# Kernel tuning notes

Hardware: AMD Instinct MI355X
Metric: run time of the kernel (lower is better)

Reference implementation:

```python
import jax, jax.numpy as jnp
import numpy as np

LN_EPS = 1e-5


def conv2d(x, w, b, stride, pad):
    # x: NCHW, w: OIHW
    y = jax.lax.conv_general_dilated(
        x, w, (stride, stride), [(pad, pad), (pad, pad)],
        dimension_numbers=("NCHW", "OIHW", "NCHW"))
    return y + b[None, :, None, None]


def gdn(x, gamma, beta):
    # y_c = x_c / sqrt(beta_c + sum_j gamma_cj * x_j^2)  (1x1 conv on x^2)
    norm = jnp.einsum("bchw,dc->bdhw", x * x, gamma) + beta[None, :, None, None]
    return x / jnp.sqrt(norm)


def layernorm(x, w, b):
    mu = jnp.mean(x, axis=-1, keepdims=True)
    var = jnp.var(x, axis=-1, keepdims=True)
    return (x - mu) / jnp.sqrt(var + LN_EPS) * w + b


def setup_inputs() -> dict:
    key = jax.random.key(0)
    ks = jax.random.split(key, 16)
    r = lambda i, shape: (jax.random.normal(ks[i], shape) * 0.02).astype(jnp.float32)
    N, M, K, D = 128, 192, 192, 128
    return {
        "x_p": jax.random.normal(ks[0], (4, 16, 3, 64, 64), jnp.float32),
        "y_g": jax.random.normal(ks[1], (64, K, 32), jnp.float32),
        "conv1_w": r(2, (N, 3, 5, 5)), "conv1_b": jnp.zeros((N,), jnp.float32),
        "gamma1": (0.1 * jnp.eye(N) + 1e-3).astype(jnp.float32), "beta1": jnp.ones((N,), jnp.float32),
        "conv2_w": r(3, (N, N, 5, 5)), "conv2_b": jnp.zeros((N,), jnp.float32),
        "gamma2": (0.1 * jnp.eye(N) + 1e-3).astype(jnp.float32), "beta2": jnp.ones((N,), jnp.float32),
        "conv3_w": r(4, (M, N, 3, 3)), "conv3_b": jnp.zeros((M,), jnp.float32),
        "ln_q_w": jnp.ones((M,), jnp.float32), "ln_q_b": jnp.zeros((M,), jnp.float32),
        "ln_kv_w": jnp.ones((K,), jnp.float32), "ln_kv_b": jnp.zeros((K,), jnp.float32),
        "ln_out_w": jnp.ones((M,), jnp.float32), "ln_out_b": jnp.zeros((M,), jnp.float32),
        "Wq": r(5, (D, M)), "Wk": r(6, (D, K)), "v_w": r(7, (1, D)),
        "Wv": r(8, (M, K)), "out_w": r(9, (M, M)), "out_b": jnp.zeros((M,), jnp.float32),
    }


def reference(x_p, y_g, conv1_w, conv1_b, gamma1, beta1, conv2_w, conv2_b,
              gamma2, beta2, conv3_w, conv3_b, ln_q_w, ln_q_b, ln_kv_w, ln_kv_b,
              ln_out_w, ln_out_b, Wq, Wk, v_w, Wv, out_w, out_b):
    B, P, C, Hp, Wp = x_p.shape
    x = x_p.reshape(B * P, C, Hp, Wp)
    # local encoder: conv s2 -> GDN -> conv s2 -> GDN -> conv s1 k3
    x = gdn(conv2d(x, conv1_w, conv1_b, 2, 2), gamma1, beta1)
    x = gdn(conv2d(x, conv2_w, conv2_b, 2, 2), gamma2, beta2)
    y_local = conv2d(x, conv3_w, conv3_b, 1, 1)          # (BP, M, h, w)
    BP, M, h, w = y_local.shape
    q = y_local.reshape(BP, M, h * w).transpose(0, 2, 1)  # (BP, Tq, M)
    kv = y_g.reshape(BP, y_g.shape[1], -1).transpose(0, 2, 1)  # (BP, Tk, K)
    q = layernorm(q, ln_q_w, ln_q_b)
    kv = layernorm(kv, ln_kv_w, ln_kv_b)
    # Bahdanau additive attention
    q_proj = jnp.einsum("bqm,dm->bqd", q, Wq)            # (BP, Tq, D)
    k_proj = jnp.einsum("bkc,dc->bkd", kv, Wk)           # (BP, Tk, D)
    energy = jnp.einsum("bqkd,d->bqk",
                        jnp.tanh(q_proj[:, :, None, :] + k_proj[:, None, :, :]),
                        v_w[0])                           # (BP, Tq, Tk)
    alpha = jax.nn.softmax(energy, axis=-1)
    v_proj = jnp.einsum("bkc,mc->bkm", kv, Wv)           # (BP, Tk, M)
    context = jnp.einsum("bqk,bkm->bqm", alpha, v_proj)
    context = jnp.einsum("bqm,nm->bqn", context, out_w) + out_b
    fused = layernorm(q + context, ln_out_w, ln_out_b)
    return fused.transpose(0, 2, 1).reshape(BP, M, h, w)
```

## Files before the change

kernel.cpp:

```cpp
#include <hip/hip_runtime.h>
#include <cstddef>
#include <cstdint>


typedef __bf16 bf16x8 __attribute__((ext_vector_type(8)));
typedef float floatx4 __attribute__((ext_vector_type(4)));
typedef unsigned short ushortT;
typedef unsigned short ushort8v __attribute__((ext_vector_type(8)));

#if __has_builtin(__builtin_amdgcn_exp2f)
#define EXP2F(x) __builtin_amdgcn_exp2f(x)
#else
#define EXP2F(x) exp2f(x)
#endif
#if __has_builtin(__builtin_amdgcn_rcpf)
#define RCPF(x) __builtin_amdgcn_rcpf(x)
#else
#define RCPF(x) (1.f / (x))
#endif

__device__ __forceinline__ ushortT f2bf(float f) {
  unsigned u = __builtin_bit_cast(unsigned, f);
  unsigned r = (u + 0x7FFFu + ((u >> 16) & 1u)) >> 16;
  return (ushortT)r;
}
__device__ __forceinline__ float bf2f(ushortT u) {
  return __builtin_bit_cast(float, ((unsigned)u) << 16);
}

static constexpr size_t OFF_T1BF = 0;
static constexpr size_t OFF_X2BF = 4194304;
static constexpr size_t OFF_T2BF = 8388608;
static constexpr size_t OFF_X3BF = 9437184;
static constexpr size_t OFF_QRAW = 10485760;
static constexpr size_t OFF_WBQ  = 21299200;
static constexpr size_t OFF_WBK  = 21311488;
static constexpr size_t OFF_WBV  = 21323776;
static constexpr size_t OFF_WBO  = 21342208;
static constexpr size_t OFF_WT2  = 26079232;
static constexpr size_t OFF_WT3  = 26284032;
static constexpr size_t OFF_WC1  = 26394624;
static constexpr size_t OFF_GB1  = 26406912;
static constexpr size_t OFF_GB2  = 26415104;

__device__ __constant__ int d_TWI2[4][9] = {{ 0, 2, 4,10,12,14,20,22,24},
                                            { 1, 3,11,13,21,23, 0, 0, 0},
                                            { 5, 7, 9,15,17,19, 0, 0, 0},
                                            { 6, 8,16,18, 0, 0, 0, 0, 0}};
__device__ __constant__ int d_NT2[4] = {9, 6, 6, 4};

__device__ void dev_convw3(const float* w, ushortT* wt, int mode, int total,
                           int idx) {
  if (idx >= total) return;
  int j    = idx & 7;
  int om   = (idx >> 3) & 63;
  int kg   = (idx >> 9) & 3;
  int slab = idx >> 11;
  int mt, s, tap, T;
  if (mode == 0) {
    int ph;
    if (slab < 72) ph = 0; else if (slab < 120) ph = 1;
    else if (slab < 168) ph = 2; else ph = 3;
    const int st[4] = {0, 72, 120, 168};
    const int ns[4] = {36, 24, 24, 16};
    int rel = slab - st[ph];
    mt = rel / ns[ph]; s = rel % ns[ph];
    tap = d_TWI2[ph][s >> 2]; T = 25;
  } else {
    mt = slab / 36; s = slab % 36; tap = s >> 2; T = 9;
  }
  int cc = s & 3;
  int c  = cc * 32 + kg * 8 + j;
  int oc = mt * 64 + om;
  wt[idx] = f2bf(w[(size_t)(oc * 128 + c) * T + tap]);
}

__device__ void dev_convw1(const float* w, ushortT* wt, int idx) {
  if (idx >= 20480) return;
  int k    = idx & 31;
  int oc   = (idx >> 5) & 127;
  int slab = idx >> 12;
  int ph, i;
  if (slab < 2) { ph = 0; i = slab; } else { ph = slab - 1; i = 0; }
  int kg = k >> 3, jj = k & 7;
  int tidx = i * 8 + jj;
  float val = 0.f;
  if (kg < 3 && tidx < d_NT2[ph]) {
    int tap = d_TWI2[ph][tidx];
    val = w[(size_t)(oc * 3 + kg) * 25 + tap];
  }
  wt[idx] = f2bf(val);
}

__device__ void dev_wcast(const float* w, ushortT* wb, int total, float scale,
                          int idx) {
  if (idx < total) wb[idx] = f2bf(w[idx] * scale);
}

__global__ __launch_bounds__(256) void prep_kernel(
    const float* __restrict__ conv2_w, ushortT* __restrict__ wt2,
    const float* __restrict__ conv3_w, ushortT* __restrict__ wt3,
    const float* __restrict__ conv1_w, ushortT* __restrict__ wc1,
    const float* __restrict__ Wq, ushortT* __restrict__ wbq,
    const float* __restrict__ Wk, ushortT* __restrict__ wbk,
    const float* __restrict__ Wv, ushortT* __restrict__ wbv,
    const float* __restrict__ out_w, ushortT* __restrict__ wbo,
    const float* __restrict__ gamma1, ushortT* __restrict__ gb1,
    const float* __restrict__ gamma2, ushortT* __restrict__ gb2) {
  constexpr float C2LE = 2.88539008177792681f;
  int blk = blockIdx.x, tid = threadIdx.x;
  if (blk < 1600)      dev_convw3(conv2_w, wt2, 0, 409600, blk * 256 + tid);
  else if (blk < 2464) dev_convw3(conv3_w, wt3, 1, 221184, (blk - 1600) * 256 + tid);
  else if (blk < 2544) dev_convw1(conv1_w, wc1, (blk - 2464) * 256 + tid);
  else if (blk < 2640) dev_wcast(Wq, wbq, 24576, C2LE, (blk - 2544) * 256 + tid);
  else if (blk < 2736) dev_wcast(Wk, wbk, 24576, C2LE, (blk - 2640) * 256 + tid);
  else if (blk < 2880) dev_wcast(Wv, wbv, 36864, 1.f, (blk - 2736) * 256 + tid);
  else if (blk < 3024) dev_wcast(out_w, wbo, 36864, 1.f, (blk - 2880) * 256 + tid);
  else if (blk < 3088) dev_wcast(gamma1, gb1, 16384, 1.f, (blk - 3024) * 256 + tid);
  else                 dev_wcast(gamma2, gb2, 16384, 1.f, (blk - 3088) * 256 + tid);
}

__global__ __launch_bounds__(256, 1) void conv1_mfma_kernel(
    const float* __restrict__ x, const ushortT* __restrict__ wc1,
    const float* __restrict__ bias, ushortT* __restrict__ outb) {
  int b  = blockIdx.x >> 2;
  int yg = blockIdx.x & 3;
  int y0 = yg * 8;

  int wave = threadIdx.x >> 6;
  int lane = threadIdx.x & 63;
  int ln15 = lane & 15;
  int kg   = lane >> 4;
  int tid  = threadIdx.x;

  __shared__ ushortT simg[4680];
  __shared__ ushortT sA[5 * 128 * 40];

  for (int j = tid; j < 2340; j += 256) ((unsigned*)simg)[j] = 0u;
  __syncthreads();

  int ihBase = 2 * y0 - 2;
  const float* xb = x + (size_t)b * 3 * 4096;
  for (int j = tid; j < 960; j += 256) {
    int q = j & 15;
    int rr = j >> 4;
    int c = rr / 20, ihl = rr % 20;
    int ih = ihBase + ihl;
    if (ih >= 0 && ih < 64) {
      float4 v = *(const float4*)&xb[c * 4096 + ih * 64 + q * 4];
      int pr = ih & 1, u = ih >> 1;
      int lr = u - y0 + 1;
      int base0 = ((pr * 2 + 0) * 3 + c) * 360 + lr * 36;
      int base1 = ((pr * 2 + 1) * 3 + c) * 360 + lr * 36;
      simg[base0 + 2 * q + 1] = f2bf(v.x);
      simg[base1 + 2 * q + 1] = f2bf(v.y);
      simg[base0 + 2 * q + 2] = f2bf(v.z);
      simg[base1 + 2 * q + 2] = f2bf(v.w);
    }
  }
  for (int j = tid; j < 2560; j += 256) {
    int chunk = j & 3, row = j >> 2;
    uint4 v = *(const uint4*)&wc1[row * 32 + chunk * 8];
    *(uint4*)&sA[row * 40 + chunk * 8] = v;
  }
  __syncthreads();

  constexpr int TDR[4][9] = {{-1,-1,-1, 0, 0, 0, 1, 1, 1},
                             {-1,-1, 0, 0, 1, 1, 0, 0, 0},
                             {-1,-1,-1, 0, 0, 0, 0, 0, 0},
                             {-1,-1, 0, 0, 0, 0, 0, 0, 0}};
  constexpr int TDC[4][9] = {{-1, 0, 1,-1, 0, 1,-1, 0, 1},
                             {-1, 0,-1, 0,-1, 0, 0, 0, 0},
                             {-1, 0, 1,-1, 0, 1, 0, 0, 0},
                             {-1, 0,-1, 0, 0, 0, 0, 0, 0}};
  constexpr int NT[4]  = {9, 6, 6, 4};
  constexpr int NM[4]  = {2, 1, 1, 1};
  constexpr int SB[4]  = {0, 2, 3, 4};

  ushort8v Bf[4][5];
  #pragma unroll
  for (int ntl = 0; ntl < 4; ++ntl) {
    int ntg = wave * 4 + ntl;
    int yloc = ntg >> 1;
    int xx = (ntg & 1) * 16 + ln15;
    int lbase = (yloc + 1) * 36 + xx + 1 + kg * 360;
    #pragma unroll
    for (int ph = 0; ph < 4; ++ph) {
      int pbase = ph * 1080 + lbase;
      #pragma unroll
      for (int i = 0; i < 2; ++i) {
        if (i < NM[ph]) {
          ushort8v bv;
          #pragma unroll
          for (int j = 0; j < 8; ++j) {
            int tidx = i * 8 + j;
            if (tidx >= NT[ph]) tidx = 0;
            int off = TDR[ph][tidx] * 36 + TDC[ph][tidx];
            bv[j] = simg[pbase + off];
          }
          Bf[ntl][SB[ph] + i] = bv;
        }
      }
    }
  }

  #pragma unroll
  for (int m = 0; m < 8; ++m) {
    bf16x8 Af[5];
    #pragma unroll
    for (int s = 0; s < 5; ++s)
      Af[s] = *(const bf16x8*)&sA[(s * 128 + m * 16 + ln15) * 40 + kg * 8];
    int oc0 = m * 16 + kg * 4;
    float4 bv = *(const float4*)&bias[oc0];
    #pragma unroll
    for (int ntl = 0; ntl < 4; ++ntl) {
      floatx4 acc = (floatx4)0.f;
      #pragma unroll
      for (int s = 0; s < 5; ++s)
        acc = __builtin_amdgcn_mfma_f32_16x16x32_bf16(
            Af[s], __builtin_bit_cast(bf16x8, Bf[ntl][s]), acc, 0, 0, 0);
      int ntg = wave * 4 + ntl;
      int y = y0 + (ntg >> 1);
      int xx = (ntg & 1) * 16 + ln15;
      int p = y * 32 + xx;
      ushort4 o4 = {f2bf(acc[0] + bv.x), f2bf(acc[1] + bv.y),
                    f2bf(acc[2] + bv.z), f2bf(acc[3] + bv.w)};
      *(ushort4*)&outb[((size_t)b * 1024 + p) * 128 + oc0] = o4;
    }
  }
}

__global__ __launch_bounds__(256) void gdn_mfma_kernel(
    const ushortT* __restrict__ xbf, const ushortT* __restrict__ gb,
    const float* __restrict__ beta, ushortT* __restrict__ ybf,
    int HW, int nPixTiles, int isSplit) {
  int pt = blockIdx.x % nPixTiles;
  int b  = blockIdx.x / nPixTiles;
  int px0 = pt * 64;
  int tid = threadIdx.x;
  int wave = tid >> 6, lane = tid & 63, ln15 = lane & 15, kg = lane >> 4;

  __shared__ ushortT sG[128 * 136];
  __shared__ ushortT sX[64 * 136];

  for (int j = tid; j < 2048; j += 256) {
    int row = j >> 4, ch = j & 15;
    *(uint4*)&sG[row * 136 + ch * 8] = *(const uint4*)&gb[row * 128 + ch * 8];
  }
  for (int j = tid; j < 1024; j += 256) {
    int row = j >> 4, ch = j & 15;
    ushort8v xv = *(const ushort8v*)&xbf[((size_t)(b * HW + px0 + row)) * 128 + ch * 8];
    ushort8v sq;
    #pragma unroll
    for (int r = 0; r < 8; ++r) {
      float f = bf2f(xv[r]);
      sq[r] = f2bf(f * f);
    }
    *(ushort8v*)&sX[row * 136 + ch * 8] = sq;
  }
  __syncthreads();

  floatx4 acc[2][4];
  #pragma unroll
  for (int mi = 0; mi < 2; ++mi)
    #pragma unroll
    for (int nt = 0; nt < 4; ++nt) acc[mi][nt] = (floatx4)0.f;

  #pragma unroll
  for (int k0 = 0; k0 < 128; k0 += 32) {
    bf16x8 a0 = *(const bf16x8*)&sG[(wave * 32 + ln15) * 136 + k0 + kg * 8];
    bf16x8 a1 = *(const bf16x8*)&sG[(wave * 32 + 16 + ln15) * 136 + k0 + kg * 8];
    #pragma unroll
    for (int nt = 0; nt < 4; ++nt) {
      bf16x8 bb = *(const bf16x8*)&sX[(nt * 16 + ln15) * 136 + k0 + kg * 8];
      acc[0][nt] = __builtin_amdgcn_mfma_f32_16x16x32_bf16(a0, bb, acc[0][nt], 0, 0, 0);
      acc[1][nt] = __builtin_amdgcn_mfma_f32_16x16x32_bf16(a1, bb, acc[1][nt], 0, 0, 0);
    }
  }

  #pragma unroll
  for (int mi = 0; mi < 2; ++mi) {
    int d0 = wave * 32 + mi * 16 + kg * 4;
    float4 bt = *(const float4*)&beta[d0];
    #pragma unroll
    for (int nt = 0; nt < 4; ++nt) {
      int p = px0 + nt * 16 + ln15;
      ushort4 x4 = *(const ushort4*)&xbf[((size_t)(b * HW + p)) * 128 + d0];
      ushort4 o4;
      o4.x = f2bf(bf2f(x4.x) * rsqrtf(acc[mi][nt][0] + bt.x));
      o4.y = f2bf(bf2f(x4.y) * rsqrtf(acc[mi][nt][1] + bt.y));
      o4.z = f2bf(bf2f(x4.z) * rsqrtf(acc[mi][nt][2] + bt.z));
      o4.w = f2bf(bf2f(x4.w) * rsqrtf(acc[mi][nt][3] + bt.w));
      size_t dst;
      if (isSplit) {
        int h = p >> 5, w5 = p & 31;
        int ph = ((h & 1) << 1) | (w5 & 1);
        dst = (((size_t)b * 4 + ph) * 256 + (h >> 1) * 16 + (w5 >> 1)) * 128 + d0;
      } else {
        dst = ((size_t)b * 256 + p) * 128 + d0;
      }
      *(ushort4*)&ybf[dst] = o4;
    }
  }
}

template<int MODE>
__global__ __launch_bounds__(256, 2) void conv_mfma_kernel(
    const ushortT* __restrict__ X,
    const ushortT* __restrict__ Wt,
    const float* __restrict__ bias,
    ushortT* __restrict__ outb) {
  constexpr int OC  = (MODE == 0) ? 128 : 192;
  constexpr int NMT = OC / 64;
  constexpr int NPH = (MODE == 0) ? 4 : 1;

  int b   = blockIdx.x / (NMT * 4);
  int rem = blockIdx.x % (NMT * 4);
  int mt  = rem >> 2;
  int rs  = rem & 3;
  int r0  = rs * 4;

  int wave = threadIdx.x >> 6;
  int lane = threadIdx.x & 63;
  int ln15 = lane & 15;
  int kg   = lane >> 4;

  __shared__ ushortT simg[6 * 18 * 136];

  floatx4 acc[4];
  #pragma unroll
  for (int m = 0; m < 4; ++m) acc[m] = (floatx4)0.f;

  constexpr int NS2[4]      = {36, 24, 24, 16};
  constexpr int PHSTART2[4] = {0, 72, 120, 168};
  constexpr int TDR_2[4][9] = {{-1,-1,-1, 0, 0, 0, 1, 1, 1},
                               {-1,-1, 0, 0, 1, 1, 0, 0, 0},
                               {-1,-1,-1, 0, 0, 0, 0, 0, 0},
                               {-1,-1, 0, 0, 0, 0, 0, 0, 0}};
  constexpr int TDC_2[4][9] = {{-1, 0, 1,-1, 0, 1,-1, 0, 1},
                               {-1, 0,-1, 0,-1, 0, 0, 0, 0},
                               {-1, 0, 1,-1, 0, 1, 0, 0, 0},
                               {-1, 0,-1, 0, 0, 0, 0, 0, 0}};
  constexpr int TDR_3[9] = {-1,-1,-1, 0, 0, 0, 1, 1, 1};
  constexpr int TDC_3[9] = {-1, 0, 1,-1, 0, 1,-1, 0, 1};

  const int aoff = kg * 512 + ln15 * 8;
  uint4 apf[8][4];

  #pragma unroll
  for (int ph = 0; ph < NPH; ++ph) {
    const int NS = (MODE == 0) ? NS2[ph] : 36;
    const int slabBase = (MODE == 0) ? (PHSTART2[ph] + mt * NS2[ph]) : (mt * 36);
    const ushortT* wp0 = Wt + (size_t)slabBase * 2048 + aoff;

    __syncthreads();
    const ushortT* Xb = X + (((size_t)b * NPH + ph) * 256) * 128;
    for (int idx = threadIdx.x; idx < 1728; idx += 256) {
      int chunk = idx & 15;
      int pix = idx >> 4;
      int row = pix / 18, colm = pix - row * 18;
      int i = r0 - 1 + row, j = colm - 1;
      uint4 v = {0u, 0u, 0u, 0u};
      if (i >= 0 && i < 16 && j >= 0 && j < 16)
        v = *(const uint4*)(Xb + ((size_t)(i * 16 + j)) * 128 + chunk * 8);
      *(uint4*)&simg[(row * 18 + colm) * 136 + chunk * 8] = v;
    }
    #pragma unroll
    for (int jj = 0; jj < 8; ++jj)
      if (jj < NS) {
        #pragma unroll
        for (int m = 0; m < 4; ++m)
          apf[jj][m] = *(const uint4*)(wp0 + (size_t)jj * 2048 + m * 128);
      }
    __syncthreads();

    #pragma unroll
    for (int s0 = 0; s0 < NS; s0 += 8) {
      #pragma unroll
      for (int jj = 0; jj < 8; ++jj) {
        int s = s0 + jj;
        if (s < NS) {
          bf16x8 acur[4];
          #pragma unroll
          for (int m = 0; m < 4; ++m) acur[m] = __builtin_bit_cast(bf16x8, apf[jj][m]);
          int sp = s + 8;
          if (sp < NS) {
            #pragma unroll
            for (int m = 0; m < 4; ++m)
              apf[jj][m] = *(const uint4*)(wp0 + (size_t)sp * 2048 + m * 128);
          }
          int t  = s >> 2;
          int c0 = (s & 3) * 32;
          int dr = (MODE == 0) ? TDR_2[ph][t] : TDR_3[t];
          int dc = (MODE == 0) ? TDC_2[ph][t] : TDC_3[t];
          int lrow = wave + dr + 1;
          int lcol = ln15 + dc + 1;
          bf16x8 bfr = *(const bf16x8*)&simg[(lrow * 18 + lcol) * 136 + c0 + kg * 8];
          #pragma unroll
          for (int m = 0; m < 4; ++m)
            acc[m] = __builtin_amdgcn_mfma_f32_16x16x32_bf16(acur[m], bfr, acc[m], 0, 0, 0);
        }
      }
    }
  }

  #pragma unroll
  for (int m = 0; m < 4; ++m) {
    int mg = mt * 64 + m * 16 + kg * 4;
    float4 bv = *(const float4*)&bias[mg];
    int r = r0 + wave;
    int p = r * 16 + ln15;
    ushort4 o4 = {f2bf(acc[m][0] + bv.x), f2bf(acc[m][1] + bv.y),
                  f2bf(acc[m][2] + bv.z), f2bf(acc[m][3] + bv.w)};
    *(ushort4*)&outb[((size_t)b * 256 + p) * OC + mg] = o4;
  }
}

__global__ __launch_bounds__(256) void attn_mega_kernel(
    const ushortT* __restrict__ qrawb, const float* __restrict__ ln_q_w,
    const float* __restrict__ ln_q_b, const float* __restrict__ yg,
    const float* __restrict__ ln_kv_w, const float* __restrict__ ln_kv_b,
    const ushortT* __restrict__ wbq, const ushortT* __restrict__ wbk,
    const ushortT* __restrict__ wbv, const ushortT* __restrict__ wbo,
    const float* __restrict__ vw, const float* __restrict__ out_b,
    const float* __restrict__ ln_out_w, const float* __restrict__ ln_out_b,
    float* __restrict__ out) {
  __shared__ ushortT smem[37640];
  ushortT* sqln   = smem;
  ushortT* skv    = smem + 6400;
  float*   skvRaw = (float*)(smem + 12800);
  float*   sqpF   = (float*)(smem + 12800);
  float*   skpF   = (float*)(smem + 21248);
  ushortT* svpT   = smem + 29696;
  float*   swm    = (float*)(smem + 37376);
  float*   sS0    = (float*)(smem + 37632);
  float*   se     = (float*)(smem + 6400);
  ushortT* sctx   = smem + 12800;
  float*   sf     = (float*)(smem + 21248);

  int b  = blockIdx.x >> 3;
  int t0 = (blockIdx.x & 7) * 32;
  int tid  = threadIdx.x;
  int wave = tid >> 6;
  int lane = tid & 63;
  int ln15 = lane & 15;
  int kg   = lane >> 4;

  {
    const float4* yg4 = (const float4*)(yg + (size_t)b * 6144);
    for (int j = tid; j < 1536; j += 256) {
      float4 v = yg4[j];
      int c = j >> 3;
      int t4 = (j & 7) * 4;
      skvRaw[(t4 + 0) * 194 + c] = v.x;
      skvRaw[(t4 + 1) * 194 + c] = v.y;
      skvRaw[(t4 + 2) * 194 + c] = v.z;
      skvRaw[(t4 + 3) * 194 + c] = v.w;
    }
  }
  for (int r = wave; r < 32; r += 4) {
    const ushortT* xr = qrawb + ((size_t)(b * 256 + t0 + r)) * 192;
    float v0 = bf2f(xr[lane]), v1 = bf2f(xr[lane + 64]), v2 = bf2f(xr[lane + 128]);
    float s = v0 + v1 + v2;
    float s2 = v0 * v0 + v1 * v1 + v2 * v2;
    #pragma unroll
    for (int off = 32; off; off >>= 1) { s += __shfl_xor(s, off); s2 += __shfl_xor(s2, off); }
    float mean = s * (1.f / 192.f);
    float var = s2 * (1.f / 192.f) - mean * mean;
    float inv = rsqrtf(var + 1e-5f);
    sqln[r * 200 + lane]       = f2bf((v0 - mean) * inv * ln_q_w[lane]       + ln_q_b[lane]);
    sqln[r * 200 + lane + 64]  = f2bf((v1 - mean) * inv * ln_q_w[lane + 64]  + ln_q_b[lane + 64]);
    sqln[r * 200 + lane + 128] = f2bf((v2 - mean) * inv * ln_q_w[lane + 128] + ln_q_b[lane + 128]);
  }
  if (tid < 128) swm[tid] = -2.f * vw[tid];
  if (tid >= 128 && tid < 192) {
    int l = tid - 128;
    float s = vw[l] + vw[l + 64];
    #pragma unroll
    for (int off = 32; off; off >>= 1) s += __shfl_xor(s, off);
    if (l == 0) *sS0 = s;
  }
  __syncthreads();

  for (int r = wave; r < 32; r += 4) {
    const float* src = skvRaw + r * 194;
    float v0 = src[lane], v1 = src[lane + 64], v2 = src[lane + 128];
    float s = v0 + v1 + v2;
    float s2 = v0 * v0 + v1 * v1 + v2 * v2;
    #pragma unroll
    for (int off = 32; off; off >>= 1) { s += __shfl_xor(s, off); s2 += __shfl_xor(s2, off); }
    float mean = s * (1.f / 192.f);
    float var = s2 * (1.f / 192.f) - mean * mean;
    float inv = rsqrtf(var + 1e-5f);
    skv[r * 200 + lane]       = f2bf((v0 - mean) * inv * ln_kv_w[lane]       + ln_kv_b[lane]);
    skv[r * 200 + lane + 64]  = f2bf((v1 - mean) * inv * ln_kv_w[lane + 64]  + ln_kv_b[lane + 64]);
    skv[r * 200 + lane + 128] = f2bf((v2 - mean) * inv * ln_kv_w[lane + 128] + ln_kv_b[lane + 128]);
  }
  __syncthreads();

  for (int ti = wave; ti < 56; ti += 4) {
    floatx4 acc = (floatx4)0.f;
    if (ti < 16) {
      int rt = ti >> 3, ct = ti & 7;
      #pragma unroll
      for (int k0 = 0; k0 < 192; k0 += 32) {
        bf16x8 afr = *(const bf16x8*)&sqln[(rt * 16 + ln15) * 200 + k0 + kg * 8];
        bf16x8 bfr = *(const bf16x8*)&wbq[((size_t)(ct * 16 + ln15)) * 192 + k0 + kg * 8];
        acc = __builtin_amdgcn_mfma_f32_16x16x32_bf16(afr, bfr, acc, 0, 0, 0);
      }
      #pragma unroll
      for (int r = 0; r < 4; ++r)
        sqpF[(rt * 16 + kg * 4 + r) * 132 + ct * 16 + ln15] = acc[r];
    } else if (ti < 32) {
      int t2 = ti - 16;
      int rt = t2 >> 3, ct = t2 & 7;
      #pragma unroll
      for (int k0 = 0; k0 < 192; k0 += 32) {
        bf16x8 afr = *(const bf16x8*)&skv[(rt * 16 + ln15) * 200 + k0 + kg * 8];
        bf16x8 bfr = *(const bf16x8*)&wbk[((size_t)(ct * 16 + ln15)) * 192 + k0 + kg * 8];
        acc = __builtin_amdgcn_mfma_f32_16x16x32_bf16(afr, bfr, acc, 0, 0, 0);
      }
      #pragma unroll
      for (int r = 0; r < 4; ++r)
        skpF[(rt * 16 + kg * 4 + r) * 132 + ct * 16 + ln15] = acc[r];
    } else {
      int t2 = ti - 32;
      int rt = t2 / 12, ct = t2 % 12;
      #pragma unroll
      for (int k0 = 0; k0 < 192; k0 += 32) {
        bf16x8 afr = *(const bf16x8*)&skv[(rt * 16 + ln15) * 200 + k0 + kg * 8];
        bf16x8 bfr = *(const bf16x8*)&wbv[((size_t)(ct * 16 + ln15)) * 192 + k0 + kg * 8];
        acc = __builtin_amdgcn_mfma_f32_16x16x32_bf16(afr, bfr, acc, 0, 0, 0);
      }
      #pragma unroll
      for (int r = 0; r < 4; ++r)
        svpT[(ct * 16 + ln15) * 40 + rt * 16 + kg * 4 + r] = f2bf(acc[r]);
    }
  }
  __syncthreads();

  {
    float S0v = *sS0;
    int qq0 = tid >> 4, kc = tid & 15;
    const float4* w4 = (const float4*)swm;
    #pragma unroll
    for (int st = 0; st < 2; ++st) {
      int qq = st * 16 + qq0;
      const float4* q4 = (const float4*)&sqpF[qq * 132];
      const float4* ka = (const float4*)&skpF[kc * 132];
      const float4* kb = (const float4*)&skpF[(kc + 16) * 132];
      float acc0 = S0v, acc1 = S0v;
      #pragma unroll 8
      for (int d4 = 0; d4 < 32; ++d4) {
        float4 qv = q4[d4], k0v = ka[d4], k1v = kb[d4], wv = w4[d4];
        acc0 += wv.x * RCPF(EXP2F(qv.x + k0v.x) + 1.f);
        acc0 += wv.y * RCPF(EXP2F(qv.y + k0v.y) + 1.f);
        acc0 += wv.z * RCPF(EXP2F(qv.z + k0v.z) + 1.f);
        acc0 += wv.w * RCPF(EXP2F(qv.w + k0v.w) + 1.f);
        acc1 += wv.x * RCPF(EXP2F(qv.x + k1v.x) + 1.f);
        acc1 += wv.y * RCPF(EXP2F(qv.y + k1v.y) + 1.f);
        acc1 += wv.z * RCPF(EXP2F(qv.z + k1v.z) + 1.f);
        acc1 += wv.w * RCPF(EXP2F(qv.w + k1v.w) + 1.f);
      }
      se[qq * 36 + kc] = acc0;
      se[qq * 36 + kc + 16] = acc1;
    }
  }
  __syncthreads();

  if (tid < 32) {
    float* ser = se + tid * 36;
    float mx = -1e30f;
    for (int k = 0; k < 32; ++k) mx = fmaxf(mx, ser[k]);
    float s = 0.f;
    for (int k = 0; k < 32; ++k) { float a = __expf(ser[k] - mx); ser[k] = a; s += a; }
    float invs = 1.f / s;
    for (int k = 0; k < 32; ++k) ser[k] *= invs;
  }
  __syncthreads();

  for (int ti = wave; ti < 24; ti += 4) {
    int rt = ti / 12, ct = ti % 12;
    float4 a0 = *(const float4*)&se[(rt * 16 + ln15) * 36 + kg * 8];
    float4 a1 = *(const float4*)&se[(rt * 16 + ln15) * 36 + kg * 8 + 4];
    ushort8v au;
    au[0] = f2bf(a0.x); au[1] = f2bf(a0.y); au[2] = f2bf(a0.z); au[3] = f2bf(a0.w);
    au[4] = f2bf(a1.x); au[5] = f2bf(a1.y); au[6] = f2bf(a1.z); au[7] = f2bf(a1.w);
    bf16x8 bfr = *(const bf16x8*)&svpT[(ct * 16 + ln15) * 40 + kg * 8];
    floatx4 acc = __builtin_amdgcn_mfma_f32_16x16x32_bf16(
        __builtin_bit_cast(bf16x8, au), bfr, (floatx4)0.f, 0, 0, 0);
    #pragma unroll
    for (int r = 0; r < 4; ++r)
      sctx[(rt * 16 + kg * 4 + r) * 200 + ct * 16 + ln15] = f2bf(acc[r]);
  }
  __syncthreads();

  for (int ti = wave; ti < 24; ti += 4) {
    int rt = ti / 12, ct = ti % 12;
    floatx4 acc = (floatx4)0.f;
    #pragma unroll
    for (int k0 = 0; k0 < 192; k0 += 32) {
      bf16x8 afr = *(const bf16x8*)&sctx[(rt * 16 + ln15) * 200 + k0 + kg * 8];
      bf16x8 bfr = *(const bf16x8*)&wbo[((size_t)(ct * 16 + ln15)) * 192 + k0 + kg * 8];
      acc = __builtin_amdgcn_mfma_f32_16x16x32_bf16(afr, bfr, acc, 0, 0, 0);
    }
    float bv = out_b[ct * 16 + ln15];
    #pragma unroll
    for (int r = 0; r < 4; ++r)
      sf[(rt * 16 + kg * 4 + r) * 193 + ct * 16 + ln15] = acc[r] + bv;
  }
  __syncthreads();

  for (int rr = wave; rr < 32; rr += 4) {
    int t = t0 + rr;
    const ushortT* xr = qrawb + ((size_t)(b * 256 + t)) * 192;
    float r0_ = bf2f(xr[lane]), r1_ = bf2f(xr[lane + 64]), r2_ = bf2f(xr[lane + 128]);
    float s = r0_ + r1_ + r2_;
    float s2 = r0_ * r0_ + r1_ * r1_ + r2_ * r2_;
    #pragma unroll
    for (int off = 32; off; off >>= 1) { s += __shfl_xor(s, off); s2 += __shfl_xor(s2, off); }
    float mean = s * (1.f / 192.f);
    float var = s2 * (1.f / 192.f) - mean * mean;
    float inv = rsqrtf(var + 1e-5f);
    float q0 = (r0_ - mean) * inv * ln_q_w[lane]       + ln_q_b[lane];
    float q1 = (r1_ - mean) * inv * ln_q_w[lane + 64]  + ln_q_b[lane + 64];
    float q2 = (r2_ - mean) * inv * ln_q_w[lane + 128] + ln_q_b[lane + 128];
    float v0 = sf[rr * 193 + lane]       + q0;
    float v1 = sf[rr * 193 + lane + 64]  + q1;
    float v2 = sf[rr * 193 + lane + 128] + q2;
    float t_s = v0 + v1 + v2;
    float t_s2 = v0 * v0 + v1 * v1 + v2 * v2;
    #pragma unroll
    for (int off = 32; off; off >>= 1) { t_s += __shfl_xor(t_s, off); t_s2 += __shfl_xor(t_s2, off); }
    float m2 = t_s * (1.f / 192.f);
    float var2 = t_s2 * (1.f / 192.f) - m2 * m2;
    float inv2 = rsqrtf(var2 + 1e-5f);
    sf[rr * 193 + lane]       = (v0 - m2) * inv2 * ln_out_w[lane]       + ln_out_b[lane];
    sf[rr * 193 + lane + 64]  = (v1 - m2) * inv2 * ln_out_w[lane + 64]  + ln_out_b[lane + 64];
    sf[rr * 193 + lane + 128] = (v2 - m2) * inv2 * ln_out_w[lane + 128] + ln_out_b[lane + 128];
  }
  __syncthreads();

  for (int j = tid; j < 1536; j += 256) {
    int m = j >> 3, t4 = j & 7;
    float4 o4;
    o4.x = sf[(t4 * 4 + 0) * 193 + m];
    o4.y = sf[(t4 * 4 + 1) * 193 + m];
    o4.z = sf[(t4 * 4 + 2) * 193 + m];
    o4.w = sf[(t4 * 4 + 3) * 193 + m];
    *(float4*)&out[((size_t)(b * 192 + m)) * 256 + t0 + t4 * 4] = o4;
  }
}

extern "C" void kernel_launch(void* const* d_in, const int* in_sizes, int n_in,
                              void* d_out, int out_size, void* d_ws, size_t ws_size,
                              hipStream_t stream) {
  (void)in_sizes; (void)n_in; (void)out_size; (void)ws_size;
  const float* x_p     = (const float*)d_in[0];
  const float* y_g     = (const float*)d_in[1];
  const float* conv1_w = (const float*)d_in[2];
  const float* conv1_b = (const float*)d_in[3];
  const float* gamma1  = (const float*)d_in[4];
  const float* beta1   = (const float*)d_in[5];
  const float* conv2_w = (const float*)d_in[6];
  const float* conv2_b = (const float*)d_in[7];
  const float* gamma2  = (const float*)d_in[8];
  const float* beta2   = (const float*)d_in[9];
  const float* conv3_w = (const float*)d_in[10];
  const float* conv3_b = (const float*)d_in[11];
  const float* ln_q_w  = (const float*)d_in[12];
  const float* ln_q_b  = (const float*)d_in[13];
  const float* ln_kv_w = (const float*)d_in[14];
  const float* ln_kv_b = (const float*)d_in[15];
  const float* ln_out_w= (const float*)d_in[16];
  const float* ln_out_b= (const float*)d_in[17];
  const float* Wq      = (const float*)d_in[18];
  const float* Wk      = (const float*)d_in[19];
  const float* v_w     = (const float*)d_in[20];
  const float* Wv      = (const float*)d_in[21];
  const float* out_w   = (const float*)d_in[22];
  const float* out_b   = (const float*)d_in[23];
  float* out = (float*)d_out;
  float* ws  = (float*)d_ws;

  ushortT* t1bf  = (ushortT*)(ws + OFF_T1BF);
  ushortT* x2bf  = (ushortT*)(ws + OFF_X2BF);
  ushortT* t2bf  = (ushortT*)(ws + OFF_T2BF);
  ushortT* x3bf  = (ushortT*)(ws + OFF_X3BF);
  ushortT* qrawb = (ushortT*)(ws + OFF_QRAW);
  ushortT* wbq   = (ushortT*)(ws + OFF_WBQ);
  ushortT* wbk   = (ushortT*)(ws + OFF_WBK);
  ushortT* wbv   = (ushortT*)(ws + OFF_WBV);
  ushortT* wbo   = (ushortT*)(ws + OFF_WBO);
  ushortT* wt2   = (ushortT*)(ws + OFF_WT2);
  ushortT* wt3   = (ushortT*)(ws + OFF_WT3);
  ushortT* wc1   = (ushortT*)(ws + OFF_WC1);
  ushortT* gb1   = (ushortT*)(ws + OFF_GB1);
  ushortT* gb2   = (ushortT*)(ws + OFF_GB2);

  prep_kernel<<<3152, 256, 0, stream>>>(conv2_w, wt2, conv3_w, wt3, conv1_w, wc1,
                                        Wq, wbq, Wk, wbk, Wv, wbv, out_w, wbo,
                                        gamma1, gb1, gamma2, gb2);
  conv1_mfma_kernel<<<256, 256, 0, stream>>>(x_p, wc1, conv1_b, t1bf);
  gdn_mfma_kernel<<<1024, 256, 0, stream>>>(t1bf, gb1, beta1, x2bf, 1024, 16, 1);
  conv_mfma_kernel<0><<<512, 256, 0, stream>>>(x2bf, wt2, conv2_b, t2bf);
  gdn_mfma_kernel<<<256, 256, 0, stream>>>(t2bf, gb2, beta2, x3bf, 256, 4, 0);
  conv_mfma_kernel<1><<<768, 256, 0, stream>>>(x3bf, wt3, conv3_b, qrawb);
  attn_mega_kernel<<<512, 256, 0, stream>>>(qrawb, ln_q_w, ln_q_b, y_g,
                                            ln_kv_w, ln_kv_b, wbq, wbk, wbv,
                                            wbo, v_w, out_b, ln_out_w,
                                            ln_out_b, out);
}
```

Measured before the change: 252.5 us.

## Split KV LayerNorm/projection into its own kernel and halve attention query tiles

Moves the per-batch KV LayerNorm and the K and V projections out of the attention mega-kernel into a separate 64-block kernel. Its outputs are written to workspace, reusing the conv1 scratch region. Before, each of the 8 query-tile blocks per batch recomputed this work redundantly. The attention kernel now handles 16 queries per block across 1024 blocks, uses less shared memory, and fuses the softmax into the energy loop through shuffles. The cost is an extra kernel launch and a global-memory round trip for kp and vT, plus some MFMA steps that run with fewer tiles per wave.

```diff
diff --git a/kernel.cpp b/kernel.cpp
--- a/kernel.cpp
+++ b/kernel.cpp
@@ -42,6 +42,8 @@
 static constexpr size_t OFF_WC1  = 26394624;
 static constexpr size_t OFF_GB1  = 26406912;
 static constexpr size_t OFF_GB2  = 26415104;
+static constexpr size_t OFF_KP   = OFF_T1BF;
+static constexpr size_t OFF_VT   = OFF_T1BF + 262144;
 
 __device__ __constant__ int d_TWI2[4][9] = {{ 0, 2, 4,10,12,14,20,22,24},
                                             { 1, 3,11,13,21,23, 0, 0, 0},
@@ -416,72 +418,28 @@
   }
 }
 
-__global__ __launch_bounds__(256) void attn_mega_kernel(
-    const ushortT* __restrict__ qrawb, const float* __restrict__ ln_q_w,
-    const float* __restrict__ ln_q_b, const float* __restrict__ yg,
-    const float* __restrict__ ln_kv_w, const float* __restrict__ ln_kv_b,
-    const ushortT* __restrict__ wbq, const ushortT* __restrict__ wbk,
-    const ushortT* __restrict__ wbv, const ushortT* __restrict__ wbo,
-    const float* __restrict__ vw, const float* __restrict__ out_b,
-    const float* __restrict__ ln_out_w, const float* __restrict__ ln_out_b,
-    float* __restrict__ out) {
-  __shared__ ushortT smem[37640];
-  ushortT* sqln   = smem;
-  ushortT* skv    = smem + 6400;
-  float*   skvRaw = (float*)(smem + 12800);
-  float*   sqpF   = (float*)(smem + 12800);
-  float*   skpF   = (float*)(smem + 21248);
-  ushortT* svpT   = smem + 29696;
-  float*   swm    = (float*)(smem + 37376);
-  float*   sS0    = (float*)(smem + 37632);
-  float*   se     = (float*)(smem + 6400);
-  ushortT* sctx   = smem + 12800;
-  float*   sf     = (float*)(smem + 21248);
-
-  int b  = blockIdx.x >> 3;
-  int t0 = (blockIdx.x & 7) * 32;
-  int tid  = threadIdx.x;
-  int wave = tid >> 6;
-  int lane = tid & 63;
-  int ln15 = lane & 15;
-  int kg   = lane >> 4;
-
-  {
-    const float4* yg4 = (const float4*)(yg + (size_t)b * 6144);
-    for (int j = tid; j < 1536; j += 256) {
-      float4 v = yg4[j];
-      int c = j >> 3;
-      int t4 = (j & 7) * 4;
-      skvRaw[(t4 + 0) * 194 + c] = v.x;
-      skvRaw[(t4 + 1) * 194 + c] = v.y;
-      skvRaw[(t4 + 2) * 194 + c] = v.z;
-      skvRaw[(t4 + 3) * 194 + c] = v.w;
-    }
-  }
-  for (int r = wave; r < 32; r += 4) {
-    const ushortT* xr = qrawb + ((size_t)(b * 256 + t0 + r)) * 192;
-    float v0 = bf2f(xr[lane]), v1 = bf2f(xr[lane + 64]), v2 = bf2f(xr[lane + 128]);
-    float s = v0 + v1 + v2;
-    float s2 = v0 * v0 + v1 * v1 + v2 * v2;
-    #pragma unroll
-    for (int off = 32; off; off >>= 1) { s += __shfl_xor(s, off); s2 += __shfl_xor(s2, off); }
-    float mean = s * (1.f / 192.f);
-    float var = s2 * (1.f / 192.f) - mean * mean;
-    float inv = rsqrtf(var + 1e-5f);
-    sqln[r * 200 + lane]       = f2bf((v0 - mean) * inv * ln_q_w[lane]       + ln_q_b[lane]);
-    sqln[r * 200 + lane + 64]  = f2bf((v1 - mean) * inv * ln_q_w[lane + 64]  + ln_q_b[lane + 64]);
-    sqln[r * 200 + lane + 128] = f2bf((v2 - mean) * inv * ln_q_w[lane + 128] + ln_q_b[lane + 128]);
-  }
-  if (tid < 128) swm[tid] = -2.f * vw[tid];
-  if (tid >= 128 && tid < 192) {
-    int l = tid - 128;
-    float s = vw[l] + vw[l + 64];
-    #pragma unroll
-    for (int off = 32; off; off >>= 1) s += __shfl_xor(s, off);
-    if (l == 0) *sS0 = s;
-  }
-  __syncthreads();
-
+__global__ __launch_bounds__(256) void kv_prep_kernel(
+    const float* __restrict__ yg, const float* __restrict__ ln_kv_w,
+    const float* __restrict__ ln_kv_b, const ushortT* __restrict__ wbk,
+    const ushortT* __restrict__ wbv, float* __restrict__ kp,
+    ushortT* __restrict__ vT) {
+  __shared__ float skvRaw[32 * 194];
+  __shared__ ushortT skv[32 * 200];
+  int b = blockIdx.x;
+  int tid = threadIdx.x;
+  int wave = tid >> 6, lane = tid & 63, ln15 = lane & 15, kg = lane >> 4;
+
+  const float4* yg4 = (const float4*)(yg + (size_t)b * 6144);
+  for (int j = tid; j < 1536; j += 256) {
+    float4 v = yg4[j];
+    int c = j >> 3;
+    int t4 = (j & 7) * 4;
+    skvRaw[(t4 + 0) * 194 + c] = v.x;
+    skvRaw[(t4 + 1) * 194 + c] = v.y;
+    skvRaw[(t4 + 2) * 194 + c] = v.z;
+    skvRaw[(t4 + 3) * 194 + c] = v.w;
+  }
+  __syncthreads();
   for (int r = wave; r < 32; r += 4) {
     const float* src = skvRaw + r * 194;
     float v0 = src[lane], v1 = src[lane + 64], v2 = src[lane + 128];
@@ -497,23 +455,10 @@
     skv[r * 200 + lane + 128] = f2bf((v2 - mean) * inv * ln_kv_w[lane + 128] + ln_kv_b[lane + 128]);
   }
   __syncthreads();
-
-  for (int ti = wave; ti < 56; ti += 4) {
+  for (int ti = wave; ti < 40; ti += 4) {
     floatx4 acc = (floatx4)0.f;
     if (ti < 16) {
       int rt = ti >> 3, ct = ti & 7;
-      #pragma unroll
-      for (int k0 = 0; k0 < 192; k0 += 32) {
-        bf16x8 afr = *(const bf16x8*)&sqln[(rt * 16 + ln15) * 200 + k0 + kg * 8];
-        bf16x8 bfr = *(const bf16x8*)&wbq[((size_t)(ct * 16 + ln15)) * 192 + k0 + kg * 8];
-        acc = __builtin_amdgcn_mfma_f32_16x16x32_bf16(afr, bfr, acc, 0, 0, 0);
-      }
-      #pragma unroll
-      for (int r = 0; r < 4; ++r)
-        sqpF[(rt * 16 + kg * 4 + r) * 132 + ct * 16 + ln15] = acc[r];
-    } else if (ti < 32) {
-      int t2 = ti - 16;
-      int rt = t2 >> 3, ct = t2 & 7;
       #pragma unroll
       for (int k0 = 0; k0 < 192; k0 += 32) {
         bf16x8 afr = *(const bf16x8*)&skv[(rt * 16 + ln15) * 200 + k0 + kg * 8];
@@ -522,9 +467,9 @@
       }
       #pragma unroll
       for (int r = 0; r < 4; ++r)
-        skpF[(rt * 16 + kg * 4 + r) * 132 + ct * 16 + ln15] = acc[r];
+        kp[((size_t)b * 32 + rt * 16 + kg * 4 + r) * 128 + ct * 16 + ln15] = acc[r];
     } else {
-      int t2 = ti - 32;
+      int t2 = ti - 16;
       int rt = t2 / 12, ct = t2 % 12;
       #pragma unroll
       for (int k0 = 0; k0 < 192; k0 += 32) {
@@ -534,84 +479,147 @@
       }
       #pragma unroll
       for (int r = 0; r < 4; ++r)
-        svpT[(ct * 16 + ln15) * 40 + rt * 16 + kg * 4 + r] = f2bf(acc[r]);
-    }
+        vT[((size_t)b * 192 + ct * 16 + ln15) * 32 + rt * 16 + kg * 4 + r] = f2bf(acc[r]);
+    }
+  }
+}
+
+__global__ __launch_bounds__(256) void attn_kernel(
+    const ushortT* __restrict__ qrawb, const float* __restrict__ ln_q_w,
+    const float* __restrict__ ln_q_b, const float* __restrict__ kp,
+    const ushortT* __restrict__ vT, const ushortT* __restrict__ wbq,
+    const ushortT* __restrict__ wbo, const float* __restrict__ vw,
+    const float* __restrict__ out_b, const float* __restrict__ ln_out_w,
+    const float* __restrict__ ln_out_b, float* __restrict__ out) {
+  __shared__ ushortT smem[17284];
+  ushortT* sqln = smem;
+  float*   skp  = (float*)(smem + 3200);
+  float*   sqpF = (float*)(smem + 11648);
+  float*   se   = (float*)(smem + 15872);
+  float*   swm  = (float*)(smem + 17024);
+  float*   sS0  = (float*)(smem + 17280);
+  ushortT* sctx = smem;
+  float*   sf   = (float*)(smem + 3200);
+
+  int b  = blockIdx.x >> 4;
+  int t0 = (blockIdx.x & 15) * 16;
+  int tid  = threadIdx.x;
+  int wave = tid >> 6;
+  int lane = tid & 63;
+  int ln15 = lane & 15;
+  int kg   = lane >> 4;
+
+  {
+    const float4* kp4 = (const float4*)(kp + (size_t)b * 4096);
+    for (int j = tid; j < 1024; j += 256) {
+      int row = j >> 5, c4 = j & 31;
+      *(float4*)&skp[row * 132 + c4 * 4] = kp4[j];
+    }
+  }
+  for (int r = wave; r < 16; r += 4) {
+    const ushortT* xr = qrawb + ((size_t)(b * 256 + t0 + r)) * 192;
+    float v0 = bf2f(xr[lane]), v1 = bf2f(xr[lane + 64]), v2 = bf2f(xr[lane + 128]);
+    float s = v0 + v1 + v2;
+    float s2 = v0 * v0 + v1 * v1 + v2 * v2;
+    #pragma unroll
+    for (int off = 32; off; off >>= 1) { s += __shfl_xor(s, off); s2 += __shfl_xor(s2, off); }
+    float mean = s * (1.f / 192.f);
+    float var = s2 * (1.f / 192.f) - mean * mean;
+    float inv = rsqrtf(var + 1e-5f);
+    sqln[r * 200 + lane]       = f2bf((v0 - mean) * inv * ln_q_w[lane]       + ln_q_b[lane]);
+    sqln[r * 200 + lane + 64]  = f2bf((v1 - mean) * inv * ln_q_w[lane + 64]  + ln_q_b[lane + 64]);
+    sqln[r * 200 + lane + 128] = f2bf((v2 - mean) * inv * ln_q_w[lane + 128] + ln_q_b[lane + 128]);
+  }
+  if (tid < 128) swm[tid] = -2.f * vw[tid];
+  if (tid >= 128 && tid < 192) {
+    int l = tid - 128;
+    float s = vw[l] + vw[l + 64];
+    #pragma unroll
+    for (int off = 32; off; off >>= 1) s += __shfl_xor(s, off);
+    if (l == 0) *sS0 = s;
+  }
+  __syncthreads();
+
+  for (int ti = wave; ti < 8; ti += 4) {
+    floatx4 acc = (floatx4)0.f;
+    #pragma unroll
+    for (int k0 = 0; k0 < 192; k0 += 32) {
+      bf16x8 afr = *(const bf16x8*)&sqln[ln15 * 200 + k0 + kg * 8];
+      bf16x8 bfr = *(const bf16x8*)&wbq[((size_t)(ti * 16 + ln15)) * 192 + k0 + kg * 8];
+      acc = __builtin_amdgcn_mfma_f32_16x16x32_bf16(afr, bfr, acc, 0, 0, 0);
+    }
+    #pragma unroll
+    for (int r = 0; r < 4; ++r)
+      sqpF[(kg * 4 + r) * 132 + ti * 16 + ln15] = acc[r];
   }
   __syncthreads();
 
   {
     float S0v = *sS0;
-    int qq0 = tid >> 4, kc = tid & 15;
+    int qq = tid >> 4, kc = tid & 15;
     const float4* w4 = (const float4*)swm;
-    #pragma unroll
-    for (int st = 0; st < 2; ++st) {
-      int qq = st * 16 + qq0;
-      const float4* q4 = (const float4*)&sqpF[qq * 132];
-      const float4* ka = (const float4*)&skpF[kc * 132];
-      const float4* kb = (const float4*)&skpF[(kc + 16) * 132];
-      float acc0 = S0v, acc1 = S0v;
-      #pragma unroll 8
-      for (int d4 = 0; d4 < 32; ++d4) {
-        float4 qv = q4[d4], k0v = ka[d4], k1v = kb[d4], wv = w4[d4];
-        acc0 += wv.x * RCPF(EXP2F(qv.x + k0v.x) + 1.f);
-        acc0 += wv.y * RCPF(EXP2F(qv.y + k0v.y) + 1.f);
-        acc0 += wv.z * RCPF(EXP2F(qv.z + k0v.z) + 1.f);
-        acc0 += wv.w * RCPF(EXP2F(qv.w + k0v.w) + 1.f);
-        acc1 += wv.x * RCPF(EXP2F(qv.x + k1v.x) + 1.f);
-        acc1 += wv.y * RCPF(EXP2F(qv.y + k1v.y) + 1.f);
-        acc1 += wv.z * RCPF(EXP2F(qv.z + k1v.z) + 1.f);
-        acc1 += wv.w * RCPF(EXP2F(qv.w + k1v.w) + 1.f);
-      }
-      se[qq * 36 + kc] = acc0;
-      se[qq * 36 + kc + 16] = acc1;
-    }
-  }
-  __syncthreads();
-
-  if (tid < 32) {
-    float* ser = se + tid * 36;
-    float mx = -1e30f;
-    for (int k = 0; k < 32; ++k) mx = fmaxf(mx, ser[k]);
-    float s = 0.f;
-    for (int k = 0; k < 32; ++k) { float a = __expf(ser[k] - mx); ser[k] = a; s += a; }
-    float invs = 1.f / s;
-    for (int k = 0; k < 32; ++k) ser[k] *= invs;
-  }
-  __syncthreads();
-
-  for (int ti = wave; ti < 24; ti += 4) {
-    int rt = ti / 12, ct = ti % 12;
-    float4 a0 = *(const float4*)&se[(rt * 16 + ln15) * 36 + kg * 8];
-    float4 a1 = *(const float4*)&se[(rt * 16 + ln15) * 36 + kg * 8 + 4];
+    const float4* q4 = (const float4*)&sqpF[qq * 132];
+    const float4* ka = (const float4*)&skp[kc * 132];
+    const float4* kb = (const float4*)&skp[(kc + 16) * 132];
+    float acc0 = S0v, acc1 = S0v;
+    #pragma unroll 8
+    for (int d4 = 0; d4 < 32; ++d4) {
+      float4 qv = q4[d4], k0v = ka[d4], k1v = kb[d4], wv = w4[d4];
+      acc0 += wv.x * RCPF(EXP2F(qv.x + k0v.x) + 1.f);
+      acc0 += wv.y * RCPF(EXP2F(qv.y + k0v.y) + 1.f);
+      acc0 += wv.z * RCPF(EXP2F(qv.z + k0v.z) + 1.f);
+      acc0 += wv.w * RCPF(EXP2F(qv.w + k0v.w) + 1.f);
+      acc1 += wv.x * RCPF(EXP2F(qv.x + k1v.x) + 1.f);
+      acc1 += wv.y * RCPF(EXP2F(qv.y + k1v.y) + 1.f);
+      acc1 += wv.z * RCPF(EXP2F(qv.z + k1v.z) + 1.f);
+      acc1 += wv.w * RCPF(EXP2F(qv.w + k1v.w) + 1.f);
+    }
+    float mx = fmaxf(acc0, acc1);
+    #pragma unroll
+    for (int off = 8; off; off >>= 1) mx = fmaxf(mx, __shfl_xor(mx, off));
+    float e0 = __expf(acc0 - mx), e1 = __expf(acc1 - mx);
+    float s = e0 + e1;
+    #pragma unroll
+    for (int off = 8; off; off >>= 1) s += __shfl_xor(s, off);
+    float inv = 1.f / s;
+    se[qq * 36 + kc]      = e0 * inv;
+    se[qq * 36 + kc + 16] = e1 * inv;
+  }
+  __syncthreads();
+
+  {
+    float4 a0 = *(const float4*)&se[ln15 * 36 + kg * 8];
+    float4 a1 = *(const float4*)&se[ln15 * 36 + kg * 8 + 4];
     ushort8v au;
     au[0] = f2bf(a0.x); au[1] = f2bf(a0.y); au[2] = f2bf(a0.z); au[3] = f2bf(a0.w);
     au[4] = f2bf(a1.x); au[5] = f2bf(a1.y); au[6] = f2bf(a1.z); au[7] = f2bf(a1.w);
-    bf16x8 bfr = *(const bf16x8*)&svpT[(ct * 16 + ln15) * 40 + kg * 8];
-    floatx4 acc = __builtin_amdgcn_mfma_f32_16x16x32_bf16(
-        __builtin_bit_cast(bf16x8, au), bfr, (floatx4)0.f, 0, 0, 0);
+    for (int ti = wave; ti < 12; ti += 4) {
+      bf16x8 bfr = *(const bf16x8*)&vT[((size_t)(b * 192 + ti * 16 + ln15)) * 32 + kg * 8];
+      floatx4 acc = __builtin_amdgcn_mfma_f32_16x16x32_bf16(
+          __builtin_bit_cast(bf16x8, au), bfr, (floatx4)0.f, 0, 0, 0);
+      #pragma unroll
+      for (int r = 0; r < 4; ++r)
+        sctx[(kg * 4 + r) * 200 + ti * 16 + ln15] = f2bf(acc[r]);
+    }
+  }
+  __syncthreads();
+
+  for (int ti = wave; ti < 12; ti += 4) {
+    floatx4 acc = (floatx4)0.f;
+    #pragma unroll
+    for (int k0 = 0; k0 < 192; k0 += 32) {
+      bf16x8 afr = *(const bf16x8*)&sctx[ln15 * 200 + k0 + kg * 8];
+      bf16x8 bfr = *(const bf16x8*)&wbo[((size_t)(ti * 16 + ln15)) * 192 + k0 + kg * 8];
+      acc = __builtin_amdgcn_mfma_f32_16x16x32_bf16(afr, bfr, acc, 0, 0, 0);
+    }
+    float bv = out_b[ti * 16 + ln15];
     #pragma unroll
     for (int r = 0; r < 4; ++r)
-      sctx[(rt * 16 + kg * 4 + r) * 200 + ct * 16 + ln15] = f2bf(acc[r]);
-  }
-  __syncthreads();
-
-  for (int ti = wave; ti < 24; ti += 4) {
-    int rt = ti / 12, ct = ti % 12;
-    floatx4 acc = (floatx4)0.f;
-    #pragma unroll
-    for (int k0 = 0; k0 < 192; k0 += 32) {
-      bf16x8 afr = *(const bf16x8*)&sctx[(rt * 16 + ln15) * 200 + k0 + kg * 8];
-      bf16x8 bfr = *(const bf16x8*)&wbo[((size_t)(ct * 16 + ln15)) * 192 + k0 + kg * 8];
-      acc = __builtin_amdgcn_mfma_f32_16x16x32_bf16(afr, bfr, acc, 0, 0, 0);
-    }
-    float bv = out_b[ct * 16 + ln15];
-    #pragma unroll
-    for (int r = 0; r < 4; ++r)
-      sf[(rt * 16 + kg * 4 + r) * 193 + ct * 16 + ln15] = acc[r] + bv;
-  }
-  __syncthreads();
-
-  for (int rr = wave; rr < 32; rr += 4) {
+      sf[(kg * 4 + r) * 193 + ti * 16 + ln15] = acc[r] + bv;
+  }
+  __syncthreads();
+
+  for (int rr = wave; rr < 16; rr += 4) {
     int t = t0 + rr;
     const ushortT* xr = qrawb + ((size_t)(b * 256 + t)) * 192;
     float r0_ = bf2f(xr[lane]), r1_ = bf2f(xr[lane + 64]), r2_ = bf2f(xr[lane + 128]);
@@ -641,8 +649,8 @@
   }
   __syncthreads();
 
-  for (int j = tid; j < 1536; j += 256) {
-    int m = j >> 3, t4 = j & 7;
+  for (int j = tid; j < 768; j += 256) {
+    int m = j >> 2, t4 = j & 3;
     float4 o4;
     o4.x = sf[(t4 * 4 + 0) * 193 + m];
     o4.y = sf[(t4 * 4 + 1) * 193 + m];
@@ -697,6 +705,8 @@
   ushortT* wc1   = (ushortT*)(ws + OFF_WC1);
   ushortT* gb1   = (ushortT*)(ws + OFF_GB1);
   ushortT* gb2   = (ushortT*)(ws + OFF_GB2);
+  float*   kp    = (float*)(ws + OFF_KP);
+  ushortT* vTb   = (ushortT*)(ws + OFF_VT);
 
   prep_kernel<<<3152, 256, 0, stream>>>(conv2_w, wt2, conv3_w, wt3, conv1_w, wc1,
                                         Wq, wbq, Wk, wbk, Wv, wbv, out_w, wbo,
@@ -706,8 +716,9 @@
   conv_mfma_kernel<0><<<512, 256, 0, stream>>>(x2bf, wt2, conv2_b, t2bf);
   gdn_mfma_kernel<<<256, 256, 0, stream>>>(t2bf, gb2, beta2, x3bf, 256, 4, 0);
   conv_mfma_kernel<1><<<768, 256, 0, stream>>>(x3bf, wt3, conv3_b, qrawb);
-  attn_mega_kernel<<<512, 256, 0, stream>>>(qrawb, ln_q_w, ln_q_b, y_g,
-                                            ln_kv_w, ln_kv_b, wbq, wbk, wbv,
-                                            wbo, v_w, out_b, ln_out_w,
-                                            ln_out_b, out);
-}
+  kv_prep_kernel<<<64, 256, 0, stream>>>(y_g, ln_kv_w, ln_kv_b, wbk, wbv,
+                                         kp, vTb);
+  attn_kernel<<<1024, 256, 0, stream>>>(qrawb, ln_q_w, ln_q_b, kp, vTb,
+                                        wbq, wbo, v_w, out_b, ln_out_w,
+                                        ln_out_b, out);
+}
```

Measured after the change: 241.0 us. 1.05x faster.
